# Optimization experiments

Hardware: AMD Instinct MI355X
Metric: run time of the kernel (lower is better)

## Reference

```python
import jax, jax.numpy as jnp
import numpy as np

N_NODES = 50000


def _gcn_norm(edge_index, num_nodes):
    # PyG GCNConv default: add self-loops, symmetric normalization D^-1/2 A D^-1/2
    row, col = edge_index[0], edge_index[1]
    loop = jnp.arange(num_nodes, dtype=edge_index.dtype)
    row = jnp.concatenate([row, loop])
    col = jnp.concatenate([col, loop])
    deg = jax.ops.segment_sum(jnp.ones_like(col, dtype=jnp.float32), col,
                              num_segments=num_nodes)
    deg_inv_sqrt = jnp.where(deg > 0, jax.lax.rsqrt(deg), 0.0)
    norm = deg_inv_sqrt[row] * deg_inv_sqrt[col]  # [E + N]
    return row, col, norm


def _gcn_conv(x, row, col, norm, W, b):
    h = x @ W                                   # [N, out]
    msg = h[row] * norm[:, None]                # gather + scale, [E+N, out]
    out = jax.ops.segment_sum(msg, col, num_segments=x.shape[0])  # scatter-add
    return out + b


def setup_inputs() -> dict:
    key = jax.random.key(0)
    k_x, k_e, k_w1, k_w2 = jax.random.split(key, 4)
    n, e, d = N_NODES, 800000, 64
    x = jax.random.normal(k_x, (n, d), dtype=jnp.float32)
    edge_index = jax.random.randint(k_e, (2, e), 0, n, dtype=jnp.int64)
    # Glorot init like PyG's Linear inside GCNConv (bias separate, zero-init here as randn-small)
    s1 = (6.0 / (d + d)) ** 0.5
    W1 = jax.random.uniform(k_w1, (d, d), jnp.float32, -s1, s1)
    W2 = jax.random.uniform(k_w2, (d, d), jnp.float32, -s1, s1)
    b1 = jnp.zeros((d,), jnp.float32)
    b2 = jnp.zeros((d,), jnp.float32)
    return {"x": x, "edge_index": edge_index, "W1": W1, "b1": b1, "W2": W2, "b2": b2}


def reference(x, edge_index, W1, b1, W2, b2):
    row, col, norm = _gcn_norm(edge_index, x.shape[0])
    h = _gcn_conv(x, row, col, norm, W1, b1)   # layer 1: in -> out
    h = _gcn_conv(h, row, col, norm, W2, b2)   # layer 2: out -> out
    return h
```

## Files before the change

kernel.cpp:

```cpp
#include <hip/hip_runtime.h>
#include <hip/hip_fp16.h>

#define DD 64
#define BSH 6
#define BNODES 64
#define NSUB 8
#define SCAP 256
#define BCAP 1536
#define TSH 14

__global__ __launch_bounds__(256) void k_zero(int4* __restrict__ p, int n4) {
    int i = blockIdx.x * 256 + threadIdx.x;
    if (i < n4) p[i] = make_int4(0, 0, 0, 0);
}

__global__ __launch_bounds__(256) void k_fill3(const int* __restrict__ rowi,
                                               const int* __restrict__ coli,
                                               int* __restrict__ cur,
                                               unsigned int* __restrict__ pk, int E) {
    int i = blockIdx.x * 256 + threadIdx.x;
    if (i < E) {
        int c = coli[i];
        int idx = (c >> BSH) * NSUB + (blockIdx.x & (NSUB - 1));
        int p = atomicAdd(&cur[idx * 16], 1);
        if (p < SCAP)
            pk[(size_t)idx * SCAP + p] =
                (unsigned int)rowi[i] | ((unsigned int)(c & (BNODES - 1)) << 16);
    }
}

__global__ __launch_bounds__(256) void k_bsortmm(const int* __restrict__ cur,
                                                 const unsigned int* __restrict__ pk,
                                                 int* __restrict__ off_s,
                                                 int* __restrict__ off_e,
                                                 float* __restrict__ dis,
                                                 int* __restrict__ srt,
                                                 const float* __restrict__ X,
                                                 const float* __restrict__ W,
                                                 __half* __restrict__ H, int n) {
    __shared__ unsigned int stage[NSUB * SCAP];
    __shared__ float xs[BNODES * 65];
    __shared__ int cnt[256];
    __shared__ int cbase[256];
    __shared__ int sb[NSUB + 1];
    __shared__ int wsum[4];
    __shared__ float sdis[BNODES];
    const int t = threadIdx.x;
    const int b = blockIdx.x;
    const int c0 = b * BNODES;

    cnt[t] = 0;
    if (t < NSUB) {
        int v = cur[(b * NSUB + t) * 16];
        if (v > SCAP) v = SCAP;
        int x = v;
#pragma unroll
        for (int d = 1; d < NSUB; d <<= 1) {
            int u = __shfl_up(x, d, NSUB);
            if ((t & (NSUB - 1)) >= d) x += u;
        }
        sb[t + 1] = x;
        if (t == 0) sb[0] = 0;
    }
    __syncthreads();
    int tot = sb[NSUB];

#pragma unroll
    for (int s = 0; s < NSUB; ++s) {
        int q0 = sb[s], len = sb[s + 1] - q0;
        const unsigned int* src = pk + ((size_t)b * NSUB + s) * SCAP;
        for (int i = t; i < len; i += 256) stage[q0 + i] = src[i];
    }
    {
        const float4* X4 = (const float4*)X;
        for (int idx = t; idx < BNODES * 16; idx += 256) {
            int row = idx >> 4, q = idx & 15, c = c0 + row;
            float4 v = make_float4(0.f, 0.f, 0.f, 0.f);
            if (c < n) v = X4[(size_t)c * 16 + q];
            int base = row * 65 + q * 4;
            xs[base + 0] = v.x; xs[base + 1] = v.y;
            xs[base + 2] = v.z; xs[base + 3] = v.w;
        }
    }
    __syncthreads();

    for (int i = t; i < tot; i += 256) {
        unsigned int k = stage[i];
        int key = (int)((k >> 16) << 2) | (int)((k & 0xFFFFu) >> TSH);
        atomicAdd(&cnt[key], 1);
    }
    __syncthreads();

    {
        const int lane = t & 63, w = t >> 6;
        int v = cnt[t], s = v;
#pragma unroll
        for (int d = 1; d < 64; d <<= 1) {
            int u = __shfl_up(s, d);
            if (lane >= d) s += u;
        }
        if (lane == 63) wsum[w] = s;
        __syncthreads();
        if (t == 0) {
            int a = 0;
#pragma unroll
            for (int q = 0; q < 4; ++q) { int tmp = wsum[q]; wsum[q] = a; a += tmp; }
        }
        __syncthreads();
        cbase[t] = wsum[w] + s - v;
    }
    __syncthreads();

    if (t < BNODES) {
        int st  = cbase[t << 2];
        int deg = cnt[(t << 2)] + cnt[(t << 2) | 1] + cnt[(t << 2) | 2] + cnt[(t << 2) | 3];
        float dv = rsqrtf((float)(deg + 1));
        sdis[t] = dv;
        int c = c0 + t;
        if (c < n) {
            off_s[c] = b * BCAP + st;
            off_e[c] = b * BCAP + st + deg;
            dis[c] = dv;
        }
    }
    __syncthreads();

    int sbeg = b * BCAP;
    for (int i = t; i < tot; i += 256) {
        unsigned int k = stage[i];
        int key = (int)((k >> 16) << 2) | (int)((k & 0xFFFFu) >> TSH);
        int pos = atomicAdd(&cbase[key], 1);
        srt[sbeg + pos] = (int)(k & 0xFFFFu);
    }
    __syncthreads();

    const int lane  = t & 63;
    const int jbase = __builtin_amdgcn_readfirstlane((t >> 6) * 16);
    float acc[16];
#pragma unroll
    for (int j = 0; j < 16; ++j) acc[j] = 0.f;
#pragma unroll 1
    for (int kc = 0; kc < 16; ++kc) {
#pragma unroll
        for (int u = 0; u < 4; ++u) {
            float sk = xs[lane * 65 + kc * 4 + u];
            const float* Wk = W + (kc * 4 + u) * 64 + jbase;
#pragma unroll
            for (int j = 0; j < 16; ++j)
                acc[j] = fmaf(sk, Wk[j], acc[j]);
        }
    }
    int c = c0 + lane;
    if (c < n) {
        float d = sdis[lane];
        __half2 hh[8];
#pragma unroll
        for (int q = 0; q < 8; ++q)
            hh[q] = __floats2half2_rn(acc[2 * q] * d, acc[2 * q + 1] * d);
        uint4* dst = (uint4*)(H + (size_t)c * DD + jbase);
        const uint4* src = (const uint4*)hh;
        dst[0] = src[0];
        dst[1] = src[1];
    }
}

__device__ __forceinline__ void gather16(const int* __restrict__ srt,
                                         const __half2* __restrict__ hv,
                                         int s, int e, int j, int hsel,
                                         float& ax, float& ay) {
    for (int p = s; p < e; p += 16) {
        int rr[16];
#pragma unroll
        for (int k = 0; k < 16; ++k)
            rr[k] = srt[min(p + k, e - 1)];
        float2 f[8];
#pragma unroll
        for (int k = 0; k < 8; ++k) {
            int ra = hsel ? rr[2 * k + 1] : rr[2 * k];
            f[k] = __half22float2(hv[(size_t)ra * 32 + j]);
        }
#pragma unroll
        for (int k = 0; k < 8; ++k) {
            bool live = (p + 2 * k + hsel) < e;
            ax += live ? f[k].x : 0.f;
            ay += live ? f[k].y : 0.f;
        }
    }
}

__global__ __launch_bounds__(256) void k_aggmm(const int* __restrict__ off_s,
                                               const int* __restrict__ off_e,
                                               const int* __restrict__ srt,
                                               const float* __restrict__ dis,
                                               const __half* __restrict__ hs,
                                               const float* __restrict__ bias1,
                                               const float* __restrict__ W2,
                                               __half* __restrict__ hs2, int n) {
    __shared__ float wld[4096];
    __shared__ float srow[4][72];
    const int t = threadIdx.x;

    {
        const float4* W4 = (const float4*)W2;
        float4* wl4 = (float4*)wld;
#pragma unroll
        for (int q = 0; q < 4; ++q) wl4[t + 256 * q] = W4[t + 256 * q];
    }
    __syncthreads();

    const int lane = t & 63;
    const int wv   = t >> 6;
    const int j    = lane & 31;
    const int hsel = lane >> 5;
    int c = __builtin_amdgcn_readfirstlane(blockIdx.x * 4 + wv);
    if (c >= n) return;

    int s = __builtin_amdgcn_readfirstlane(off_s[c]);
    int e = __builtin_amdgcn_readfirstlane(off_e[c]);
    float d = dis[c];

    const __half2* hv = (const __half2*)hs;

    float ax = 0.f, ay = 0.f;
    if (hsel == 0) {
        float2 f = __half22float2(hv[(size_t)c * 32 + j]);
        ax = f.x; ay = f.y;
    }
    gather16(srt, hv, s, e, j, hsel, ax, ay);
    ax += __shfl_xor(ax, 32);
    ay += __shfl_xor(ay, 32);

    if (hsel == 0) {
        float2 bb = ((const float2*)bias1)[j];
        srow[wv][2 * j]     = bb.x + d * ax;
        srow[wv][2 * j + 1] = bb.y + d * ay;
    }
    __builtin_amdgcn_wave_barrier();

    float acc = 0.f;
#pragma unroll 8
    for (int k = 0; k < 64; ++k)
        acc = fmaf(srow[wv][k], wld[k * 64 + lane], acc);
    hs2[(size_t)c * DD + lane] = __float2half(d * acc);
}

__global__ __launch_bounds__(256) void k_agg(const int* __restrict__ off_s,
                                             const int* __restrict__ off_e,
                                             const int* __restrict__ srt,
                                             const float* __restrict__ dis,
                                             const __half* __restrict__ hs,
                                             const float* __restrict__ bias,
                                             float* __restrict__ outf, int n) {
    int lane = threadIdx.x & 63;
    int j    = lane & 31;
    int hsel = lane >> 5;
    int c = __builtin_amdgcn_readfirstlane(blockIdx.x * 4 + (threadIdx.x >> 6));
    if (c >= n) return;

    int s = __builtin_amdgcn_readfirstlane(off_s[c]);
    int e = __builtin_amdgcn_readfirstlane(off_e[c]);

    const __half2* hv = (const __half2*)hs;

    float ax = 0.f, ay = 0.f;
    if (hsel == 0) {
        float2 f = __half22float2(hv[(size_t)c * 32 + j]);
        ax = f.x; ay = f.y;
    }
    gather16(srt, hv, s, e, j, hsel, ax, ay);
    ax += __shfl_xor(ax, 32);
    ay += __shfl_xor(ay, 32);
    if (hsel == 0) {
        float d = dis[c];
        float2 bb = ((const float2*)bias)[j];
        ((float2*)outf)[(size_t)c * 32 + j] = make_float2(bb.x + d * ax, bb.y + d * ay);
    }
}

extern "C" void kernel_launch(void* const* d_in, const int* in_sizes, int n_in,
                              void* d_out, int out_size, void* d_ws, size_t ws_size,
                              hipStream_t stream) {
    const float* x  = (const float*)d_in[0];
    const int*   ei = (const int*)d_in[1];
    const float* W1 = (const float*)d_in[2];
    const float* b1 = (const float*)d_in[3];
    const float* W2 = (const float*)d_in[4];
    const float* b2 = (const float*)d_in[5];
    float* out = (float*)d_out;

    int n = in_sizes[0] / DD;
    int E = in_sizes[1] / 2;
    const int* rowi = ei;
    const int* coli = ei + E;
    int nb = (n + BNODES - 1) / BNODES;
    int M  = nb * NSUB;

    char* ws = (char*)d_ws;
    int*          cur   = (int*)ws;
    int*          off_s = (int*)(ws + (size_t)1024 * 1024);
    int*          off_e = (int*)(ws + (size_t)1280 * 1024);
    float*        dis   = (float*)(ws + (size_t)1536 * 1024);
    unsigned int* pk    = (unsigned int*)(ws + (size_t)2048 * 1024);
    int*          srt   = (int*)(ws + (size_t)9216 * 1024);
    __half*       hs1   = (__half*)(ws + (size_t)14336 * 1024);
    __half*       hs2   = (__half*)(ws + (size_t)21504 * 1024);

    int n4    = M * 4;
    int nb_z  = (n4 + 255) / 256;
    int nb_e  = (E + 255) / 256;
    int nb_ag = (n + 3) / 4;

    k_zero   <<<nb_z, 256, 0, stream>>>((int4*)cur, n4);
    k_fill3  <<<nb_e, 256, 0, stream>>>(rowi, coli, cur, pk, E);
    k_bsortmm<<<nb, 256, 0, stream>>>(cur, pk, off_s, off_e, dis, srt, x, W1, hs1, n);

    k_aggmm<<<nb_ag, 256, 0, stream>>>(off_s, off_e, srt, dis, hs1, b1, W2, hs2, n);

    k_agg<<<nb_ag, 256, 0, stream>>>(off_s, off_e, srt, dis, hs2, b2, out, n);
}
```

Before: 121.5 us.

## Split half-precision features into two 32-column planes and stage neighbor indices in LDS

Stores the fp16 hidden features as two separate 32-column arrays, so each gathered neighbor row is 64 bytes. Aggregation now runs two passes, one per half, with 4 neighbors per wave step (16 lanes each) instead of 2. Neighbor indices (up to 96) are staged once in shared memory and reused by both passes. The intent is a smaller footprint per gather pass for better cache hit rates, at the cost of loading each edge index twice and running more gather loop iterations.

```diff
diff --git a/kernel.cpp b/kernel.cpp
--- a/kernel.cpp
+++ b/kernel.cpp
@@ -8,6 +8,7 @@
 #define SCAP 256
 #define BCAP 1536
 #define TSH 14
+#define DCAPMAX 96
 
 __global__ __launch_bounds__(256) void k_zero(int4* __restrict__ p, int n4) {
     int i = blockIdx.x * 256 + threadIdx.x;
@@ -37,7 +38,8 @@
                                                  int* __restrict__ srt,
                                                  const float* __restrict__ X,
                                                  const float* __restrict__ W,
-                                                 __half* __restrict__ H, int n) {
+                                                 __half* __restrict__ hsA,
+                                                 __half* __restrict__ hsB, int n) {
     __shared__ unsigned int stage[NSUB * SCAP];
     __shared__ float xs[BNODES * 65];
     __shared__ int cnt[256];
@@ -157,34 +159,49 @@
 #pragma unroll
         for (int q = 0; q < 8; ++q)
             hh[q] = __floats2half2_rn(acc[2 * q] * d, acc[2 * q + 1] * d);
-        uint4* dst = (uint4*)(H + (size_t)c * DD + jbase);
+        __half* base = (jbase < 32) ? hsA : hsB;
+        uint4* dst = (uint4*)(base + (size_t)c * 32 + (jbase & 31));
         const uint4* src = (const uint4*)hh;
         dst[0] = src[0];
         dst[1] = src[1];
     }
 }
 
-__device__ __forceinline__ void gather16(const int* __restrict__ srt,
-                                         const __half2* __restrict__ hv,
-                                         int s, int e, int j, int hsel,
-                                         float& ax, float& ay) {
-    for (int p = s; p < e; p += 16) {
-        int rr[16];
-#pragma unroll
-        for (int k = 0; k < 16; ++k)
-            rr[k] = srt[min(p + k, e - 1)];
-        float2 f[8];
-#pragma unroll
-        for (int k = 0; k < 8; ++k) {
-            int ra = hsel ? rr[2 * k + 1] : rr[2 * k];
-            f[k] = __half22float2(hv[(size_t)ra * 32 + j]);
-        }
-#pragma unroll
-        for (int k = 0; k < 8; ++k) {
-            bool live = (p + 2 * k + hsel) < e;
-            ax += live ? f[k].x : 0.f;
-            ay += live ? f[k].y : 0.f;
-        }
+__device__ __forceinline__ void gather_phase(const int* sidx_w,
+                                             const int* __restrict__ srt_g,
+                                             const __half2* __restrict__ hp,
+                                             int c, int deg, int dcap,
+                                             int j, int hsel,
+                                             float& ax, float& ay) {
+    ax = 0.f; ay = 0.f;
+    if (hsel == 0) {
+        float2 f = __half22float2(hp[(size_t)c * 16 + j]);
+        ax = f.x; ay = f.y;
+    }
+    int p = 0;
+    for (; p + 16 <= dcap; p += 16) {
+        int i0 = sidx_w[p + hsel];
+        int i1 = sidx_w[p + 4 + hsel];
+        int i2 = sidx_w[p + 8 + hsel];
+        int i3 = sidx_w[p + 12 + hsel];
+        float2 f0 = __half22float2(hp[(size_t)i0 * 16 + j]);
+        float2 f1 = __half22float2(hp[(size_t)i1 * 16 + j]);
+        float2 f2 = __half22float2(hp[(size_t)i2 * 16 + j]);
+        float2 f3 = __half22float2(hp[(size_t)i3 * 16 + j]);
+        ax += (f0.x + f1.x) + (f2.x + f3.x);
+        ay += (f0.y + f1.y) + (f2.y + f3.y);
+    }
+    for (; p < dcap; p += 4) {
+        int q = p + hsel;
+        int idx = sidx_w[min(q, dcap - 1)];
+        float2 f = __half22float2(hp[(size_t)idx * 16 + j]);
+        bool live = q < dcap;
+        ax += live ? f.x : 0.f;
+        ay += live ? f.y : 0.f;
+    }
+    for (int q = dcap + hsel; q < deg; q += 4) {
+        float2 f = __half22float2(hp[(size_t)srt_g[q] * 16 + j]);
+        ax += f.x; ay += f.y;
     }
 }
 
@@ -192,12 +209,15 @@
                                                const int* __restrict__ off_e,
                                                const int* __restrict__ srt,
                                                const float* __restrict__ dis,
-                                               const __half* __restrict__ hs,
+                                               const __half* __restrict__ hA,
+                                               const __half* __restrict__ hB,
                                                const float* __restrict__ bias1,
                                                const float* __restrict__ W2,
-                                               __half* __restrict__ hs2, int n) {
+                                               __half* __restrict__ oA,
+                                               __half* __restrict__ oB, int n) {
     __shared__ float wld[4096];
     __shared__ float srow[4][72];
+    __shared__ int sidx[4][DCAPMAX];
     const int t = threadIdx.x;
 
     {
@@ -210,30 +230,36 @@
 
     const int lane = t & 63;
     const int wv   = t >> 6;
-    const int j    = lane & 31;
-    const int hsel = lane >> 5;
+    const int j    = lane & 15;
+    const int hsel = lane >> 4;
     int c = __builtin_amdgcn_readfirstlane(blockIdx.x * 4 + wv);
     if (c >= n) return;
 
     int s = __builtin_amdgcn_readfirstlane(off_s[c]);
     int e = __builtin_amdgcn_readfirstlane(off_e[c]);
+    int deg = e - s, dcap = min(deg, DCAPMAX);
     float d = dis[c];
 
-    const __half2* hv = (const __half2*)hs;
-
-    float ax = 0.f, ay = 0.f;
-    if (hsel == 0) {
-        float2 f = __half22float2(hv[(size_t)c * 32 + j]);
-        ax = f.x; ay = f.y;
-    }
-    gather16(srt, hv, s, e, j, hsel, ax, ay);
-    ax += __shfl_xor(ax, 32);
-    ay += __shfl_xor(ay, 32);
-
-    if (hsel == 0) {
-        float2 bb = ((const float2*)bias1)[j];
+    for (int i = lane; i < dcap; i += 64) sidx[wv][i] = srt[s + i];
+    __builtin_amdgcn_wave_barrier();
+
+    float ax, ay;
+    float2 bb;
+    gather_phase(sidx[wv], srt + s, (const __half2*)hA, c, deg, dcap, j, hsel, ax, ay);
+    ax += __shfl_xor(ax, 16); ay += __shfl_xor(ay, 16);
+    ax += __shfl_xor(ax, 32); ay += __shfl_xor(ay, 32);
+    if (hsel == 0) {
+        bb = ((const float2*)bias1)[j];
         srow[wv][2 * j]     = bb.x + d * ax;
         srow[wv][2 * j + 1] = bb.y + d * ay;
+    }
+    gather_phase(sidx[wv], srt + s, (const __half2*)hB, c, deg, dcap, j, hsel, ax, ay);
+    ax += __shfl_xor(ax, 16); ay += __shfl_xor(ay, 16);
+    ax += __shfl_xor(ax, 32); ay += __shfl_xor(ay, 32);
+    if (hsel == 0) {
+        bb = ((const float2*)(bias1 + 32))[j];
+        srow[wv][32 + 2 * j] = bb.x + d * ax;
+        srow[wv][33 + 2 * j] = bb.y + d * ay;
     }
     __builtin_amdgcn_wave_barrier();
 
@@ -241,39 +267,50 @@
 #pragma unroll 8
     for (int k = 0; k < 64; ++k)
         acc = fmaf(srow[wv][k], wld[k * 64 + lane], acc);
-    hs2[(size_t)c * DD + lane] = __float2half(d * acc);
+    __half hv = __float2half(d * acc);
+    if (lane < 32) oA[(size_t)c * 32 + lane] = hv;
+    else           oB[(size_t)c * 32 + (lane - 32)] = hv;
 }
 
 __global__ __launch_bounds__(256) void k_agg(const int* __restrict__ off_s,
                                              const int* __restrict__ off_e,
                                              const int* __restrict__ srt,
                                              const float* __restrict__ dis,
-                                             const __half* __restrict__ hs,
+                                             const __half* __restrict__ hA,
+                                             const __half* __restrict__ hB,
                                              const float* __restrict__ bias,
                                              float* __restrict__ outf, int n) {
-    int lane = threadIdx.x & 63;
-    int j    = lane & 31;
-    int hsel = lane >> 5;
-    int c = __builtin_amdgcn_readfirstlane(blockIdx.x * 4 + (threadIdx.x >> 6));
+    __shared__ int sidx[4][DCAPMAX];
+    const int t = threadIdx.x;
+    const int lane = t & 63;
+    const int wv   = t >> 6;
+    const int j    = lane & 15;
+    const int hsel = lane >> 4;
+    int c = __builtin_amdgcn_readfirstlane(blockIdx.x * 4 + wv);
     if (c >= n) return;
 
     int s = __builtin_amdgcn_readfirstlane(off_s[c]);
     int e = __builtin_amdgcn_readfirstlane(off_e[c]);
-
-    const __half2* hv = (const __half2*)hs;
-
-    float ax = 0.f, ay = 0.f;
-    if (hsel == 0) {
-        float2 f = __half22float2(hv[(size_t)c * 32 + j]);
-        ax = f.x; ay = f.y;
-    }
-    gather16(srt, hv, s, e, j, hsel, ax, ay);
-    ax += __shfl_xor(ax, 32);
-    ay += __shfl_xor(ay, 32);
-    if (hsel == 0) {
-        float d = dis[c];
+    int deg = e - s, dcap = min(deg, DCAPMAX);
+    float d = dis[c];
+
+    for (int i = lane; i < dcap; i += 64) sidx[wv][i] = srt[s + i];
+    __builtin_amdgcn_wave_barrier();
+
+    float ax, ay;
+    gather_phase(sidx[wv], srt + s, (const __half2*)hA, c, deg, dcap, j, hsel, ax, ay);
+    ax += __shfl_xor(ax, 16); ay += __shfl_xor(ay, 16);
+    ax += __shfl_xor(ax, 32); ay += __shfl_xor(ay, 32);
+    if (hsel == 0) {
         float2 bb = ((const float2*)bias)[j];
         ((float2*)outf)[(size_t)c * 32 + j] = make_float2(bb.x + d * ax, bb.y + d * ay);
+    }
+    gather_phase(sidx[wv], srt + s, (const __half2*)hB, c, deg, dcap, j, hsel, ax, ay);
+    ax += __shfl_xor(ax, 16); ay += __shfl_xor(ay, 16);
+    ax += __shfl_xor(ax, 32); ay += __shfl_xor(ay, 32);
+    if (hsel == 0) {
+        float2 bb = ((const float2*)(bias + 32))[j];
+        ((float2*)outf)[(size_t)c * 32 + 16 + j] = make_float2(bb.x + d * ax, bb.y + d * ay);
     }
 }
 
@@ -302,8 +339,10 @@
     float*        dis   = (float*)(ws + (size_t)1536 * 1024);
     unsigned int* pk    = (unsigned int*)(ws + (size_t)2048 * 1024);
     int*          srt   = (int*)(ws + (size_t)9216 * 1024);
-    __half*       hs1   = (__half*)(ws + (size_t)14336 * 1024);
-    __half*       hs2   = (__half*)(ws + (size_t)21504 * 1024);
+    __half*       h1A   = (__half*)(ws + (size_t)14336 * 1024);
+    __half*       h1B   = (__half*)(ws + (size_t)17664 * 1024);
+    __half*       h2A   = (__half*)(ws + (size_t)20992 * 1024);
+    __half*       h2B   = (__half*)(ws + (size_t)24320 * 1024);
 
     int n4    = M * 4;
     int nb_z  = (n4 + 255) / 256;
@@ -312,9 +351,11 @@
 
     k_zero   <<<nb_z, 256, 0, stream>>>((int4*)cur, n4);
     k_fill3  <<<nb_e, 256, 0, stream>>>(rowi, coli, cur, pk, E);
-    k_bsortmm<<<nb, 256, 0, stream>>>(cur, pk, off_s, off_e, dis, srt, x, W1, hs1, n);
-
-    k_aggmm<<<nb_ag, 256, 0, stream>>>(off_s, off_e, srt, dis, hs1, b1, W2, hs2, n);
-
-    k_agg<<<nb_ag, 256, 0, stream>>>(off_s, off_e, srt, dis, hs2, b2, out, n);
-}
+    k_bsortmm<<<nb, 256, 0, stream>>>(cur, pk, off_s, off_e, dis, srt, x, W1,
+                                      h1A, h1B, n);
+
+    k_aggmm<<<nb_ag, 256, 0, stream>>>(off_s, off_e, srt, dis, h1A, h1B, b1, W2,
+                                       h2A, h2B, n);
+
+    k_agg<<<nb_ag, 256, 0, stream>>>(off_s, off_e, srt, dis, h2A, h2B, b2, out, n);
+}
```

Result: slower. 139.5 us (+14.8%).
